# Performance work log

Hardware: AMD Instinct MI355X
Metric: run time of the kernel (lower is better)

Reference implementation:

```python
import jax, jax.numpy as jnp
import numpy as np
from jax.scipy.linalg import solve_triangular

N, K, D = 131072, 8, 32  # samples, clusters, dims


def setup_inputs() -> dict:
    key = jax.random.key(0)
    k1, k2, k3, k4 = jax.random.split(key, 4)
    return {
        "X": jax.random.normal(k1, (N, D), dtype=jnp.float32),
        "mu": jax.random.normal(k2, (K, D), dtype=jnp.float32),
        "L": jax.random.normal(k3, (K, D, D), dtype=jnp.float32),
        "weights": jax.random.normal(k4, (K,), dtype=jnp.float32),
        "it": 0,
    }


def _mixture_log_likelihoods(X, mu, L, weights):
    K_, D_ = mu.shape
    LOG2PI = float(np.log(2.0 * np.pi))
    # update_covariances: A_k = L_k L_k^T + I  (always SPD -> cholesky succeeds)
    A = jnp.einsum('kab,kcb->kac', L, L) + jnp.eye(D_, dtype=L.dtype)
    Lc = jnp.linalg.cholesky(A)            # [K,D,D] lower Cholesky factors
    invLc = jnp.linalg.inv(Lc)             # [K,D,D]
    # all cluster pairs (cartesian_prod order: i outer, j inner)
    ii, jj = [g.reshape(-1) for g in jnp.meshgrid(jnp.arange(K_), jnp.arange(K_), indexing='ij')]
    Si, Sj = Lc[ii], Lc[jj]                # NOTE: original uses the CHOLESKY FACTORS here
    invSi, invSj = invLc[ii], invLc[jj]
    mui, muj = mu[ii], mu[jj]
    # _gaussian_product: sigma = inv(inv(Si)+inv(Sj)); mu = sigma @ (inv(Si) mu_i + inv(Sj) mu_j)
    sigma = jnp.linalg.inv(invSi + invSj)                      # [P,D,D]
    rhs = jnp.einsum('pab,pb->pa', invSi, mui) + jnp.einsum('pab,pb->pa', invSj, muj)
    mu_p = jnp.einsum('pab,pb->pa', sigma, rhs)                # [P,D]
    # _product_z: log(1/sqrt(det(2*pi*(Si+Sj))) * exp(-0.5 dmu^T inv(Si+Sj) dmu))
    S = Si + Sj
    dmu = mui - muj
    quad = -0.5 * jnp.einsum('pa,pab,pb->p', dmu, jnp.linalg.inv(S), dmu)
    z = -0.5 * jnp.log(jnp.linalg.det(2.0 * np.pi * S)) + quad  # [P]
    # _unormalised_pdf: lower-triangular solve against sigma (only lower triangle used)
    diff = X[None, :, :] - mu_p[:, None, :]                    # [P,N,D]
    m = solve_triangular(sigma, jnp.swapaxes(diff, 1, 2), lower=True)  # [P,D,N]
    ll = -0.5 * (jnp.sum(m * m, axis=1) + D_ * LOG2PI
                 + jnp.log(jnp.linalg.det(sigma))[:, None])    # [P,N]
    logw = jax.nn.log_softmax(weights)                         # softmax weights, then log
    logprob = z[:, None] + ll + logw[ii][:, None] + logw[jj][:, None]  # [P,N]
    return jnp.log(jnp.sum(jnp.exp(logprob), axis=0))          # [N]


def reference(X, mu, L, weights, it):
    ll = _mixture_log_likelihoods(X, mu, L, weights)
    return jax.scipy.special.logsumexp(ll, axis=0)  # scalar
```

## Files before the change

kernel.cpp:

```cpp
#include <hip/hip_runtime.h>

#define D 32
#define K 8
#define NPAIR 36
#define PROWS 576

#define PMOFF 0
#define WOFF 4608
#define C2OFF 4864
#define CMAXOFF 4900
#define TICKOFF 4904
#define LCOFF 4928
#define PARTOFF 13120

typedef float v2f __attribute__((ext_vector_type(2)));

__host__ __device__ constexpr int gidx(int i, int j) {
    return i * 8 + j - i * (i + 1) / 2;
}
__host__ __device__ constexpr int proff(int r) {
    return 4 * (r / 4 + 1) * (2 * (r / 4) + (r % 4));
}

__global__ __launch_bounds__(64) void setup1_kernel(
    const float* __restrict__ mu, const float* __restrict__ L,
    float* __restrict__ ws)
{
    __shared__ float sA[D][D + 1];
    __shared__ float sLc[D][D + 1];
    __shared__ float sI[D][D + 1];
    const int k = blockIdx.x;
    const int tid = threadIdx.x;
    const int i = tid & 31;

    for (int e = tid; e < D * D; e += 64) sI[e >> 5][e & 31] = L[k * D * D + e];
    __syncthreads();

    for (int e = tid; e < D * D; e += 64) {
        const int a = e >> 5, c = e & 31;
        float s = (a == c) ? 1.0f : 0.0f;
        #pragma unroll
        for (int b = 0; b < D; ++b) s = fmaf(sI[a][b], sI[c][b], s);
        sA[a][c] = s;
    }
    __syncthreads();

    float lrow[D];
    #pragma unroll
    for (int j = 0; j < D; ++j) {
        if (i == j) {
            float s = sA[j][j];
            #pragma unroll
            for (int b = 0; b < j; ++b) s = fmaf(-lrow[b], lrow[b], s);
            const float d = sqrtf(s);
            lrow[j] = d;
            #pragma unroll
            for (int b = 0; b < j; ++b) sLc[j][b] = lrow[b];
            sLc[j][j] = d;
        }
        __syncthreads();
        if (i > j) {
            float s = sA[i][j];
            #pragma unroll
            for (int b = 0; b < j; ++b) s = fmaf(-lrow[b], sLc[j][b], s);
            lrow[j] = s / sLc[j][j];
        }
    }
    __syncthreads();

    for (int e = tid; e < D * D; e += 64) {
        const int r = e >> 5, c = e & 31;
        ws[LCOFF + k * D * D + e] = (c <= r) ? sLc[r][c] : 0.0f;
    }

    {
        const int j = i;
        #pragma unroll
        for (int ii = 0; ii < D; ++ii) {
            float s = (ii == j) ? 1.0f : 0.0f;
            #pragma unroll
            for (int b = 0; b < ii; ++b) s = fmaf(-sLc[ii][b], sI[b][j], s);
            const float cii = s / sLc[ii][ii];
            sI[ii][j] = cii;
            const int w4 = 4 * (ii / 4 + 1);
            if (j < w4) ws[PMOFF + k * PROWS + proff(ii) + j] = cii;
        }
    }
    __syncthreads();

    {
        float s = 0.0f;
        #pragma unroll
        for (int b = 0; b < D; ++b) s = fmaf(sI[i][b], mu[k * D + b], s);
        ws[WOFF + k * D + i] = s;
    }
}

#define SLC(kk, r, c) sLc2[(kk) * 1024 + (r) * 32 + (c)]

__global__ __launch_bounds__(256) void setup2_kernel(
    const float* __restrict__ mu, const float* __restrict__ weights,
    float* __restrict__ ws)
{
    __shared__ float sLc2[K * D * D];
    __shared__ float sMu[K * D];
    __shared__ float sWt[K];
    __shared__ float sLogw[K];
    __shared__ float sCp[NPAIR];
    __shared__ float sCmax;
    const int tid = threadIdx.x;

    {
        const float4* src = (const float4*)(ws + LCOFF);
        float4* dst = (float4*)sLc2;
        #pragma unroll
        for (int e = 0; e < 8; ++e) dst[tid + 256 * e] = src[tid + 256 * e];
        sMu[tid] = mu[tid];
        if (tid < K) sWt[tid] = weights[tid];
    }
    __syncthreads();

    if (tid == 0) {
        float m = -INFINITY;
        for (int t = 0; t < K; ++t) m = fmaxf(m, sWt[t]);
        float s = 0.0f;
        for (int t = 0; t < K; ++t) s += expf(sWt[t] - m);
        const float lse = m + logf(s);
        for (int t = 0; t < K; ++t) sLogw[t] = sWt[t] - lse;
        *(unsigned int*)(ws + TICKOFF) = 0u;
    }
    __syncthreads();

    if (tid < NPAIR) {
        int tt = tid, pi = 0;
        while (tt >= (K - pi)) { tt -= (K - pi); ++pi; }
        const int pj = pi + tt;
        const float LOG2PI = 1.8378770664093453f;
        float sumlogS = 0.0f, logdetsig = 0.0f;
        #pragma unroll
        for (int r = 0; r < D; ++r) {
            const float di = SLC(pi, r, r), dj = SLC(pj, r, r);
            sumlogS += logf(di + dj);
            logdetsig -= logf(1.0f / di + 1.0f / dj);
        }
        float v[D];
        float quad_acc = 0.0f;
        #pragma unroll
        for (int r = 0; r < D; ++r) {
            const float d0 = sMu[pi * D + r] - sMu[pj * D + r];
            float s = d0;
            #pragma unroll
            for (int b = 0; b < r; ++b)
                s = fmaf(-(SLC(pi, r, b) + SLC(pj, r, b)), v[b], s);
            v[r] = s / (SLC(pi, r, r) + SLC(pj, r, r));
            quad_acc = fmaf(d0, v[r], quad_acc);
        }
        const float quad = -0.5f * quad_acc;
        float c = quad - 0.5f * sumlogS - (float)D * LOG2PI - 0.5f * logdetsig
                  + sLogw[pi] + sLogw[pj];
        if (pi < pj) c += 0.6931471805599453f;
        sCp[tid] = c;
    }
    __syncthreads();
    if (tid == 0) {
        float m = -INFINITY;
        for (int t = 0; t < NPAIR; ++t) m = fmaxf(m, sCp[t]);
        sCmax = m;
        ws[CMAXOFF] = m;
    }
    __syncthreads();
    if (tid < NPAIR)
        ws[C2OFF + tid] = (sCp[tid] - sCmax) * 1.4426950408889634f;
}

__global__ __launch_bounds__(128, 2) void main_kernel(
    const float* __restrict__ X, const float* __restrict__ cst,
    float* __restrict__ partials, float* __restrict__ out,
    unsigned int* __restrict__ ticket, int nsamp, int nblk)
{
    __shared__ __align__(16) float2 sXch[NPAIR * 65];
    __shared__ int sIsLast;
    __shared__ float sRed[2];
    const int tid = threadIdx.x;
    const int wv = tid >> 6;
    const int lane = tid & 63;

    const int n0 = blockIdx.x * 128 + lane;
    const int n1 = n0 + 64;
    const int m0 = (n0 < nsamp) ? n0 : 0;
    const int m1 = (n1 < nsamp) ? n1 : 0;

    v2f xs[D];
    {
        const float4* Xv0 = (const float4*)(X + m0 * D);
        const float4* Xv1 = (const float4*)(X + m1 * D);
        #pragma unroll
        for (int q = 0; q < 8; ++q) {
            const float4 t0 = Xv0[q];
            const float4 t1 = Xv1[q];
            xs[4 * q + 0] = (v2f){t0.x, t1.x};
            xs[4 * q + 1] = (v2f){t0.y, t1.y};
            xs[4 * q + 2] = (v2f){t0.z, t1.z};
            xs[4 * q + 3] = (v2f){t0.w, t1.w};
        }
    }

    v2f G2[NPAIR];
    #pragma unroll
    for (int t = 0; t < NPAIR; ++t) G2[t] = (v2f){0.0f, 0.0f};

    #pragma unroll
    for (int rh = 0; rh < 8; ++rh) {
        if ((rh & 1) == wv) {
            #pragma unroll
            for (int rr = 0; rr < 4; ++rr) {
                const int r = 4 * rh + rr;
                v2f y2[K];
                #pragma unroll
                for (int k = 0; k < K; ++k) {
                    const float wvv = cst[WOFF + k * D + r];
                    v2f a = (v2f){-wvv, -wvv};
                    const float* Mr = cst + k * PROWS + proff(r);
                    #pragma unroll
                    for (int c4 = 0; c4 <= rh; ++c4) {
                        const float4 m4 = *(const float4*)(Mr + 4 * c4);
                        a = __builtin_elementwise_fma((v2f){m4.x, m4.x},
                                                      xs[4 * c4 + 0], a);
                        a = __builtin_elementwise_fma((v2f){m4.y, m4.y},
                                                      xs[4 * c4 + 1], a);
                        a = __builtin_elementwise_fma((v2f){m4.z, m4.z},
                                                      xs[4 * c4 + 2], a);
                        a = __builtin_elementwise_fma((v2f){m4.w, m4.w},
                                                      xs[4 * c4 + 3], a);
                    }
                    y2[k] = a;
                }
                #pragma unroll
                for (int pi = 0; pi < K; ++pi)
                    #pragma unroll
                    for (int pj = pi; pj < K; ++pj)
                        G2[gidx(pi, pj)] = __builtin_elementwise_fma(
                            y2[pi], y2[pj], G2[gidx(pi, pj)]);
            }
        }
    }

    __syncthreads();

    if (wv == 1) {
        #pragma unroll
        for (int t = 0; t < NPAIR; ++t)
            sXch[t * 65 + lane] = make_float2(G2[t].x, G2[t].y);
    }
    __syncthreads();

    if (wv == 0) {
        #pragma unroll
        for (int t = 0; t < NPAIR; ++t) {
            const float2 g = sXch[t * 65 + lane];
            G2[t] += (v2f){g.x, g.y};
        }

        v2f acc2 = (v2f){0.0f, 0.0f};
        const float NH = -0.72134752044448170f;
        #pragma unroll
        for (int pi = 0; pi < K; ++pi)
            #pragma unroll
            for (int pj = pi; pj < K; ++pj) {
                const v2f q2 = __builtin_elementwise_fma(
                    (v2f){2.0f, 2.0f}, G2[gidx(pi, pj)],
                    G2[gidx(pi, pi)] + G2[gidx(pj, pj)]);
                const float c = cst[C2OFF + gidx(pi, pj)];
                const v2f e2 = __builtin_elementwise_fma((v2f){NH, NH}, q2,
                                                         (v2f){c, c});
                acc2.x += exp2f(e2.x);
                acc2.y += exp2f(e2.y);
            }
        float acc = ((n0 < nsamp) ? acc2.x : 0.0f)
                  + ((n1 < nsamp) ? acc2.y : 0.0f);

        #pragma unroll
        for (int s = 1; s < 64; s <<= 1) acc += __shfl_xor(acc, s, 64);
        if (lane == 0) {
            partials[blockIdx.x] = acc;
            __threadfence();
            const unsigned prev = atomicAdd(ticket, 1u);
            sIsLast = (prev == (unsigned)(nblk - 1)) ? 1 : 0;
        }
    }
    __syncthreads();

    if (sIsLast) {
        __threadfence();
        float a2 = 0.0f;
        for (int e = tid; e < nblk; e += 128) a2 += partials[e];
        #pragma unroll
        for (int s = 1; s < 64; s <<= 1) a2 += __shfl_xor(a2, s, 64);
        if (lane == 0) sRed[wv] = a2;
        __syncthreads();
        if (tid == 0) out[0] = cst[CMAXOFF] + logf(sRed[0] + sRed[1]);
    }
}

extern "C" void kernel_launch(void* const* d_in, const int* in_sizes, int n_in,
                              void* d_out, int out_size, void* d_ws, size_t ws_size,
                              hipStream_t stream) {
    const float* X = (const float*)d_in[0];
    const float* mu = (const float*)d_in[1];
    const float* L = (const float*)d_in[2];
    const float* w = (const float*)d_in[3];
    float* wsf = (float*)d_ws;
    float* out = (float*)d_out;

    const int nsamp = in_sizes[0] / D;
    const int nblk = (nsamp + 127) / 128;

    setup1_kernel<<<K, 64, 0, stream>>>(mu, L, wsf);
    setup2_kernel<<<1, 256, 0, stream>>>(mu, w, wsf);
    main_kernel<<<nblk, 128, 0, stream>>>(X, wsf, wsf + PARTOFF, out,
                                          (unsigned int*)(wsf + TICKOFF),
                                          nsamp, nblk);
}
```

Before: 172.1 us.

## Compute per-cluster whitening with split-bf16 MFMA instead of scalar FMAs

```diff
diff --git a/kernel.cpp b/kernel.cpp
--- a/kernel.cpp
+++ b/kernel.cpp
@@ -3,23 +3,46 @@
 #define D 32
 #define K 8
 #define NPAIR 36
-#define PROWS 576
-
-#define PMOFF 0
-#define WOFF 4608
-#define C2OFF 4864
-#define CMAXOFF 4900
-#define TICKOFF 4904
-#define LCOFF 4928
-#define PARTOFF 13120
-
-typedef float v2f __attribute__((ext_vector_type(2)));
+
+#define AFROFF 0
+#define WFROFF 8192
+#define C2OFF 8448
+#define CMAXOFF 8484
+#define TICKOFF 8488
+#define LCOFF 8512
+#define PARTOFF 16704
+
+typedef short s16x8 __attribute__((ext_vector_type(8)));
+typedef float f32x16 __attribute__((ext_vector_type(16)));
+
+union FragU { uint4 u4; s16x8 s8; };
 
 __host__ __device__ constexpr int gidx(int i, int j) {
     return i * 8 + j - i * (i + 1) / 2;
 }
-__host__ __device__ constexpr int proff(int r) {
-    return 4 * (r / 4 + 1) * (2 * (r / 4) + (r % 4));
+
+static __device__ inline unsigned short f2bf(float v) {
+    union { float f; unsigned u; } c; c.f = v;
+    unsigned r = (c.u + 0x7FFFu + ((c.u >> 16) & 1u)) >> 16;
+    return (unsigned short)r;
+}
+static __device__ inline float bf2f(unsigned short h) {
+    union { unsigned u; float f; } c; c.u = ((unsigned)h) << 16;
+    return c.f;
+}
+
+static __device__ inline void pack8(const float* v, uint4& hi, uint4& lo) {
+    unsigned hw[4], lw[4];
+    #pragma unroll
+    for (int p = 0; p < 4; ++p) {
+        const unsigned short h0 = f2bf(v[2 * p]);
+        const unsigned short h1 = f2bf(v[2 * p + 1]);
+        hw[p] = (unsigned)h0 | ((unsigned)h1 << 16);
+        lw[p] = (unsigned)f2bf(v[2 * p] - bf2f(h0))
+              | ((unsigned)f2bf(v[2 * p + 1] - bf2f(h1)) << 16);
+    }
+    hi = make_uint4(hw[0], hw[1], hw[2], hw[3]);
+    lo = make_uint4(lw[0], lw[1], lw[2], lw[3]);
 }
 
 __global__ __launch_bounds__(64) void setup1_kernel(
@@ -29,9 +52,12 @@
     __shared__ float sA[D][D + 1];
     __shared__ float sLc[D][D + 1];
     __shared__ float sI[D][D + 1];
+    __shared__ float sWv[D];
     const int k = blockIdx.x;
     const int tid = threadIdx.x;
     const int i = tid & 31;
+    const int row = tid & 31;
+    const int hg = tid >> 5;
 
     for (int e = tid; e < D * D; e += 64) sI[e >> 5][e & 31] = L[k * D * D + e];
     __syncthreads();
@@ -80,10 +106,7 @@
             float s = (ii == j) ? 1.0f : 0.0f;
             #pragma unroll
             for (int b = 0; b < ii; ++b) s = fmaf(-sLc[ii][b], sI[b][j], s);
-            const float cii = s / sLc[ii][ii];
-            sI[ii][j] = cii;
-            const int w4 = 4 * (ii / 4 + 1);
-            if (j < w4) ws[PMOFF + k * PROWS + proff(ii) + j] = cii;
+            sI[ii][j] = s / sLc[ii][ii];
         }
     }
     __syncthreads();
@@ -92,7 +115,24 @@
         float s = 0.0f;
         #pragma unroll
         for (int b = 0; b < D; ++b) s = fmaf(sI[i][b], mu[k * D + b], s);
-        ws[WOFF + k * D + i] = s;
+        if (tid < 32) sWv[i] = s;
+    }
+
+    #pragma unroll
+    for (int s = 0; s < 2; ++s) {
+        float v[8];
+        #pragma unroll
+        for (int e = 0; e < 8; ++e) v[e] = sI[row][16 * s + 8 * hg + e];
+        uint4 hi, lo;
+        pack8(v, hi, lo);
+        *(uint4*)((char*)ws + AFROFF * 4 + k * 4096 + ((s * 2 + 0) * 64 + tid) * 16) = hi;
+        *(uint4*)((char*)ws + AFROFF * 4 + k * 4096 + ((s * 2 + 1) * 64 + tid) * 16) = lo;
+    }
+    __syncthreads();
+
+    if (tid < 32) {
+        const int h = tid >> 4, r = tid & 15;
+        ws[WFROFF + k * 32 + h * 16 + r] = -sWv[(r & 3) + 8 * (r >> 2) + 4 * h];
     }
 }
 
@@ -173,132 +213,117 @@
         ws[C2OFF + tid] = (sCp[tid] - sCmax) * 1.4426950408889634f;
 }
 
-__global__ __launch_bounds__(128, 2) void main_kernel(
+__global__ __launch_bounds__(256) void main_kernel(
     const float* __restrict__ X, const float* __restrict__ cst,
     float* __restrict__ partials, float* __restrict__ out,
     unsigned int* __restrict__ ticket, int nsamp, int nblk)
 {
-    __shared__ __align__(16) float2 sXch[NPAIR * 65];
+    __shared__ float sRed[4];
     __shared__ int sIsLast;
-    __shared__ float sRed[2];
     const int tid = threadIdx.x;
     const int wv = tid >> 6;
     const int lane = tid & 63;
-
-    const int n0 = blockIdx.x * 128 + lane;
-    const int n1 = n0 + 64;
-    const int m0 = (n0 < nsamp) ? n0 : 0;
-    const int m1 = (n1 < nsamp) ? n1 : 0;
-
-    v2f xs[D];
+    const int col = lane & 31;
+    const int hg = lane >> 5;
+
+    const int n = blockIdx.x * 128 + wv * 32 + col;
+    const int m = (n < nsamp) ? n : 0;
+
+    FragU bh0, bl0, bh1, bl1;
     {
-        const float4* Xv0 = (const float4*)(X + m0 * D);
-        const float4* Xv1 = (const float4*)(X + m1 * D);
-        #pragma unroll
-        for (int q = 0; q < 8; ++q) {
-            const float4 t0 = Xv0[q];
-            const float4 t1 = Xv1[q];
-            xs[4 * q + 0] = (v2f){t0.x, t1.x};
-            xs[4 * q + 1] = (v2f){t0.y, t1.y};
-            xs[4 * q + 2] = (v2f){t0.z, t1.z};
-            xs[4 * q + 3] = (v2f){t0.w, t1.w};
-        }
-    }
-
-    v2f G2[NPAIR];
-    #pragma unroll
-    for (int t = 0; t < NPAIR; ++t) G2[t] = (v2f){0.0f, 0.0f};
-
-    #pragma unroll
-    for (int rh = 0; rh < 8; ++rh) {
-        if ((rh & 1) == wv) {
-            #pragma unroll
-            for (int rr = 0; rr < 4; ++rr) {
-                const int r = 4 * rh + rr;
-                v2f y2[K];
-                #pragma unroll
-                for (int k = 0; k < K; ++k) {
-                    const float wvv = cst[WOFF + k * D + r];
-                    v2f a = (v2f){-wvv, -wvv};
-                    const float* Mr = cst + k * PROWS + proff(r);
-                    #pragma unroll
-                    for (int c4 = 0; c4 <= rh; ++c4) {
-                        const float4 m4 = *(const float4*)(Mr + 4 * c4);
-                        a = __builtin_elementwise_fma((v2f){m4.x, m4.x},
-                                                      xs[4 * c4 + 0], a);
-                        a = __builtin_elementwise_fma((v2f){m4.y, m4.y},
-                                                      xs[4 * c4 + 1], a);
-                        a = __builtin_elementwise_fma((v2f){m4.z, m4.z},
-                                                      xs[4 * c4 + 2], a);
-                        a = __builtin_elementwise_fma((v2f){m4.w, m4.w},
-                                                      xs[4 * c4 + 3], a);
-                    }
-                    y2[k] = a;
-                }
-                #pragma unroll
-                for (int pi = 0; pi < K; ++pi)
-                    #pragma unroll
-                    for (int pj = pi; pj < K; ++pj)
-                        G2[gidx(pi, pj)] = __builtin_elementwise_fma(
-                            y2[pi], y2[pj], G2[gidx(pi, pj)]);
-            }
-        }
-    }
-
-    __syncthreads();
-
-    if (wv == 1) {
-        #pragma unroll
-        for (int t = 0; t < NPAIR; ++t)
-            sXch[t * 65 + lane] = make_float2(G2[t].x, G2[t].y);
-    }
-    __syncthreads();
-
-    if (wv == 0) {
-        #pragma unroll
-        for (int t = 0; t < NPAIR; ++t) {
-            const float2 g = sXch[t * 65 + lane];
-            G2[t] += (v2f){g.x, g.y};
-        }
-
-        v2f acc2 = (v2f){0.0f, 0.0f};
-        const float NH = -0.72134752044448170f;
-        #pragma unroll
-        for (int pi = 0; pi < K; ++pi)
-            #pragma unroll
-            for (int pj = pi; pj < K; ++pj) {
-                const v2f q2 = __builtin_elementwise_fma(
-                    (v2f){2.0f, 2.0f}, G2[gidx(pi, pj)],
-                    G2[gidx(pi, pi)] + G2[gidx(pj, pj)]);
-                const float c = cst[C2OFF + gidx(pi, pj)];
-                const v2f e2 = __builtin_elementwise_fma((v2f){NH, NH}, q2,
-                                                         (v2f){c, c});
-                acc2.x += exp2f(e2.x);
-                acc2.y += exp2f(e2.y);
-            }
-        float acc = ((n0 < nsamp) ? acc2.x : 0.0f)
-                  + ((n1 < nsamp) ? acc2.y : 0.0f);
-
-        #pragma unroll
-        for (int s = 1; s < 64; s <<= 1) acc += __shfl_xor(acc, s, 64);
-        if (lane == 0) {
-            partials[blockIdx.x] = acc;
-            __threadfence();
-            const unsigned prev = atomicAdd(ticket, 1u);
-            sIsLast = (prev == (unsigned)(nblk - 1)) ? 1 : 0;
-        }
+        const float4 a0 = *(const float4*)(X + m * D + 8 * hg);
+        const float4 a1 = *(const float4*)(X + m * D + 8 * hg + 4);
+        const float4 a2 = *(const float4*)(X + m * D + 16 + 8 * hg);
+        const float4 a3 = *(const float4*)(X + m * D + 16 + 8 * hg + 4);
+        float v0[8] = {a0.x, a0.y, a0.z, a0.w, a1.x, a1.y, a1.z, a1.w};
+        float v1[8] = {a2.x, a2.y, a2.z, a2.w, a3.x, a3.y, a3.z, a3.w};
+        pack8(v0, bh0.u4, bl0.u4);
+        pack8(v1, bh1.u4, bl1.u4);
+    }
+
+    const char* afr = (const char*)cst;
+    const float* wfr = cst + WFROFF;
+
+    f32x16 yk[K];
+    #pragma unroll
+    for (int k = 0; k < K; ++k) {
+        FragU ah0, al0, ah1, al1;
+        ah0.u4 = *(const uint4*)(afr + k * 4096 + (0 * 64 + lane) * 16);
+        al0.u4 = *(const uint4*)(afr + k * 4096 + (1 * 64 + lane) * 16);
+        ah1.u4 = *(const uint4*)(afr + k * 4096 + (2 * 64 + lane) * 16);
+        al1.u4 = *(const uint4*)(afr + k * 4096 + (3 * 64 + lane) * 16);
+
+        f32x16 acc1;
+        {
+            const float4* wp = (const float4*)(wfr + k * 32 + hg * 16);
+            const float4 w0 = wp[0], w1 = wp[1], w2 = wp[2], w3 = wp[3];
+            acc1[0] = w0.x;  acc1[1] = w0.y;  acc1[2] = w0.z;  acc1[3] = w0.w;
+            acc1[4] = w1.x;  acc1[5] = w1.y;  acc1[6] = w1.z;  acc1[7] = w1.w;
+            acc1[8] = w2.x;  acc1[9] = w2.y;  acc1[10] = w2.z; acc1[11] = w2.w;
+            acc1[12] = w3.x; acc1[13] = w3.y; acc1[14] = w3.z; acc1[15] = w3.w;
+        }
+        f32x16 acc2 = (f32x16)(0.0f);
+
+        acc1 = __builtin_amdgcn_mfma_f32_32x32x16_bf16(ah0.s8, bh0.s8, acc1, 0, 0, 0);
+        acc2 = __builtin_amdgcn_mfma_f32_32x32x16_bf16(al1.s8, bh1.s8, acc2, 0, 0, 0);
+        acc1 = __builtin_amdgcn_mfma_f32_32x32x16_bf16(ah1.s8, bh1.s8, acc1, 0, 0, 0);
+        acc2 = __builtin_amdgcn_mfma_f32_32x32x16_bf16(ah0.s8, bl0.s8, acc2, 0, 0, 0);
+        acc1 = __builtin_amdgcn_mfma_f32_32x32x16_bf16(al0.s8, bh0.s8, acc1, 0, 0, 0);
+        acc2 = __builtin_amdgcn_mfma_f32_32x32x16_bf16(ah1.s8, bl1.s8, acc2, 0, 0, 0);
+
+        yk[k] = acc1 + acc2;
+    }
+
+    float G[NPAIR];
+    #pragma unroll
+    for (int pi = 0; pi < K; ++pi)
+        #pragma unroll
+        for (int pj = pi; pj < K; ++pj) {
+            float g = 0.0f;
+            #pragma unroll
+            for (int r = 0; r < 16; ++r)
+                g = fmaf(yk[pi][r], yk[pj][r], g);
+            G[gidx(pi, pj)] = g;
+        }
+
+    float accs = 0.0f;
+    const float NH = -0.72134752044448170f;
+    #pragma unroll
+    for (int pi = 0; pi < K; ++pi)
+        #pragma unroll
+        for (int pj = pi; pj < K; ++pj) {
+            const float q = 2.0f * G[gidx(pi, pj)]
+                          + G[gidx(pi, pi)] + G[gidx(pj, pj)];
+            const float qf = q + __shfl_xor(q, 32, 64);
+            accs += exp2f(fmaf(NH, qf, cst[C2OFF + gidx(pi, pj)]));
+        }
+    accs = (n < nsamp) ? accs : 0.0f;
+
+    #pragma unroll
+    for (int s = 1; s < 64; s <<= 1) accs += __shfl_xor(accs, s, 64);
+    if (lane == 0) sRed[wv] = 0.5f * accs;
+    __syncthreads();
+
+    if (tid == 0) {
+        const float blocksum = sRed[0] + sRed[1] + sRed[2] + sRed[3];
+        partials[blockIdx.x] = blocksum;
+        __threadfence();
+        const unsigned prev = atomicAdd(ticket, 1u);
+        sIsLast = (prev == (unsigned)(nblk - 1)) ? 1 : 0;
     }
     __syncthreads();
 
     if (sIsLast) {
         __threadfence();
         float a2 = 0.0f;
-        for (int e = tid; e < nblk; e += 128) a2 += partials[e];
+        for (int e = tid; e < nblk; e += 256) a2 += partials[e];
         #pragma unroll
         for (int s = 1; s < 64; s <<= 1) a2 += __shfl_xor(a2, s, 64);
-        if (lane == 0) sRed[wv] = a2;
+        if ((tid & 63) == 0) sRed[tid >> 6] = a2;
         __syncthreads();
-        if (tid == 0) out[0] = cst[CMAXOFF] + logf(sRed[0] + sRed[1]);
+        if (tid == 0)
+            out[0] = cst[CMAXOFF]
+                   + logf(sRed[0] + sRed[1] + sRed[2] + sRed[3]);
     }
 }
 
@@ -317,7 +342,7 @@
 
     setup1_kernel<<<K, 64, 0, stream>>>(mu, L, wsf);
     setup2_kernel<<<1, 256, 0, stream>>>(mu, w, wsf);
-    main_kernel<<<nblk, 128, 0, stream>>>(X, wsf, wsf + PARTOFF, out,
+    main_kernel<<<nblk, 256, 0, stream>>>(X, wsf, wsf + PARTOFF, out,
                                           (unsigned int*)(wsf + TICKOFF),
                                           nsamp, nblk);
 }
```

Result: faster. 151.1 us (-12.2%).
